# Optimization experiments

Measured on AMD Instinct MI355X. Metric: run time of the kernel, lower is better.

## Reference

```python
import jax, jax.numpy as jnp
import numpy as np

NUM_POINTS = 16384
OVERSAMPLE = 3
IMPORTANCE_RATIO = 0.75


def point_sample(feat, coords):
    """grid_sample(bilinear, align_corners=False, zero padding) at [0,1]^2 coords.
    feat: (N, C, H, W); coords: (N, P, 2) with coords[...,0]=x (width), [...,1]=y.
    Returns (N, C, P)."""
    N, C, H, W = feat.shape
    # grid_sample with g = 2c-1, align_corners=False -> pixel = c*size - 0.5
    x = coords[..., 0] * W - 0.5
    y = coords[..., 1] * H - 0.5
    x0 = jnp.floor(x)
    y0 = jnp.floor(y)
    x1 = x0 + 1.0
    y1 = y0 + 1.0
    wx1 = x - x0
    wx0 = 1.0 - wx1
    wy1 = y - y0
    wy0 = 1.0 - wy1
    featf = feat.reshape(N, C, H * W)

    def gather(yi, xi):
        valid = (xi >= 0) & (xi <= W - 1) & (yi >= 0) & (yi <= H - 1)
        xic = jnp.clip(xi, 0, W - 1).astype(jnp.int32)
        yic = jnp.clip(yi, 0, H - 1).astype(jnp.int32)
        idx = yic * W + xic  # (N, P)
        v = jnp.take_along_axis(featf, idx[:, None, :], axis=2)  # (N, C, P)
        return v * valid[:, None, :].astype(feat.dtype)

    out = (gather(y0, x0) * (wy0 * wx0)[:, None, :]
           + gather(y0, x1) * (wy0 * wx1)[:, None, :]
           + gather(y1, x0) * (wy1 * wx0)[:, None, :]
           + gather(y1, x1) * (wy1 * wx1)[:, None, :])
    return out


def calculate_uncertainty(logits):
    """logits: (N, C, P) -> (N, P) uncertainty = top2 - top1 (<= 0)."""
    if logits.shape[1] == 1:
        return -jnp.abs(logits)[:, 0, :]
    top2 = jax.lax.top_k(jnp.moveaxis(logits, 1, -1), 2)[0]  # (N, P, 2)
    return top2[..., 1] - top2[..., 0]


def sample_point_coords(coarse_logits):
    """get_uncertain_point_coords_with_randomness (torch.no_grad branch)."""
    N = coarse_logits.shape[0]
    num_sampled = NUM_POINTS * OVERSAMPLE
    num_imp = int(IMPORTANCE_RATIO * NUM_POINTS)
    num_rand = NUM_POINTS - num_imp
    k1, k2 = jax.random.split(jax.random.key(7))
    cand = jax.random.uniform(k1, (N, num_sampled, 2), dtype=jnp.float32)
    cand_logits = point_sample(coarse_logits, cand)  # (N, C, S)
    unc = calculate_uncertainty(cand_logits)  # (N, S)
    idx = jax.lax.top_k(unc, num_imp)[1]  # (N, num_imp)
    imp = jnp.take_along_axis(cand, idx[..., None], axis=1)  # (N, num_imp, 2)
    rand = jax.random.uniform(k2, (N, num_rand, 2), dtype=jnp.float32)
    return jnp.concatenate([imp, rand], axis=1)  # (N, P, 2)


def point_head(fine, coarse_pts, w0, b0, w1, b1, w2, b2, wp, bp):
    x = jnp.concatenate([fine, coarse_pts], axis=1)  # (N, nin+C, P)
    for w, b in ((w0, b0), (w1, b1), (w2, b2)):
        x = jax.nn.relu(jnp.einsum('oc,ncp->nop', w, x) + b[None, :, None])
        x = jnp.concatenate([x, coarse_pts], axis=1)  # coarse_pred_each_layer
    return jnp.einsum('oc,ncp->nop', wp, x) + bp[None, :, None]  # (N, C, P)


def setup_inputs() -> dict:
    key = jax.random.key(0)
    ks = jax.random.split(key, 8)
    N, C, Hc, Wc = 8, 19, 64, 64
    nin, Hf, Wf = 256, 128, 128
    fin = nin + C  # 275
    return {
        'coarse_sem_seg_logits': jax.random.normal(ks[0], (N, C, Hc, Wc), jnp.float32),
        'features': jax.random.normal(ks[1], (N, nin, Hf, Wf), jnp.float32),
        'w0': jax.random.normal(ks[2], (nin, fin), jnp.float32) * (2.0 / fin) ** 0.5,
        'b0': jnp.zeros((nin,), jnp.float32),
        'w1': jax.random.normal(ks[3], (nin, fin), jnp.float32) * (2.0 / fin) ** 0.5,
        'b1': jnp.zeros((nin,), jnp.float32),
        'w2': jax.random.normal(ks[4], (nin, fin), jnp.float32) * (2.0 / fin) ** 0.5,
        'b2': jnp.zeros((nin,), jnp.float32),
        'wp': jax.random.normal(ks[5], (C, fin), jnp.float32) * 0.001,
        'bp': jnp.zeros((C,), jnp.float32),
    }


def reference(coarse_sem_seg_logits, features, w0, b0, w1, b1, w2, b2, wp, bp):
    # training-mode forward of PointRendSemSegHead
    point_coords = jax.lax.stop_gradient(
        sample_point_coords(jax.lax.stop_gradient(coarse_sem_seg_logits)))
    coarse_pts = point_sample(coarse_sem_seg_logits, point_coords)  # (N, C, P)
    fine_pts = point_sample(features, point_coords)  # (N, nin, P)
    point_logits = point_head(fine_pts, coarse_pts, w0, b0, w1, b1, w2, b2, wp, bp)
    return coarse_sem_seg_logits, point_logits, point_coords
```

## Files before the change

### kernel.cpp

```cpp
#include <hip/hip_runtime.h>
#include <stdint.h>

#pragma clang fp contract(off)

#define NB    8
#define CCH   19
#define FCH   256
#define FIN   275
#define KP    288
#define NPTS  16384
#define NSAMP 49152
#define NIMP  12288
#define NRAND 4096
#define SORT_M 65536
#define CHUNK  8192
#define TP    64
#define XROW  640
#define WBF_OFF (4u << 20)
#define FTR_OFF (8u << 20)
#define FTR_BYTES (134217728ull / 2)

typedef __attribute__((ext_vector_type(8))) short bf16x8;
typedef __attribute__((ext_vector_type(4))) float f32x4;

__host__ __device__ __forceinline__ uint32_t rotl32(uint32_t v, int r) {
  return (v << r) | (v >> (32 - r));
}

__host__ __device__ __forceinline__ void tf2x32(uint32_t k0, uint32_t k1,
                                                uint32_t x0, uint32_t x1,
                                                uint32_t* o0, uint32_t* o1) {
  const uint32_t ks2 = k0 ^ k1 ^ 0x1BD11BDAu;
  x0 += k0; x1 += k1;
#define TF_R(r) { x0 += x1; x1 = rotl32(x1, (r)); x1 ^= x0; }
  TF_R(13) TF_R(15) TF_R(26) TF_R(6)
  x0 += k1;  x1 += ks2 + 1u;
  TF_R(17) TF_R(29) TF_R(16) TF_R(24)
  x0 += ks2; x1 += k0 + 2u;
  TF_R(13) TF_R(15) TF_R(26) TF_R(6)
  x0 += k0;  x1 += k1 + 3u;
  TF_R(17) TF_R(29) TF_R(16) TF_R(24)
  x0 += k1;  x1 += ks2 + 4u;
  TF_R(13) TF_R(15) TF_R(26) TF_R(6)
  x0 += ks2; x1 += k0 + 5u;
#undef TF_R
  *o0 = x0; *o1 = x1;
}

__device__ __forceinline__ float u01_at(uint32_t k0, uint32_t k1, uint32_t i) {
  uint32_t o0, o1;
  tf2x32(k0, k1, 0u, i, &o0, &o1);
  const uint32_t b = o0 ^ o1;
  const float f = __uint_as_float((b >> 9) | 0x3f800000u) - 1.0f;
  return fmaxf(0.0f, f);
}

__device__ __forceinline__ unsigned short f2bf(float f) {
  const uint32_t u = __float_as_uint(f);
  return (unsigned short)((u + 0x7fffu + ((u >> 16) & 1u)) >> 16);
}

__device__ __forceinline__ float bf2f(unsigned short h) {
  return __uint_as_float((uint32_t)h << 16);
}

template <int SZ>
__device__ __forceinline__ void interp(float cx, float cy, int* off, float* wgt) {
  const float X = cx * (float)SZ - 0.5f, Y = cy * (float)SZ - 0.5f;
  const float x0f = floorf(X), y0f = floorf(Y);
  const float fx = X - x0f, fy = Y - y0f;
  const float wx0 = 1.0f - fx, wy0 = 1.0f - fy;
  const int x0 = (int)x0f, y0 = (int)y0f;
  const int x0c = min(max(x0, 0), SZ - 1), x1c = min(max(x0 + 1, 0), SZ - 1);
  const int y0c = min(max(y0, 0), SZ - 1), y1c = min(max(y0 + 1, 0), SZ - 1);
  const bool vx0 = (x0 >= 0) & (x0 <= SZ - 1), vx1 = (x0 >= -1) & (x0 <= SZ - 2);
  const bool vy0 = (y0 >= 0) & (y0 <= SZ - 1), vy1 = (y0 >= -1) & (y0 <= SZ - 2);
  off[0] = y0c * SZ + x0c; wgt[0] = (vy0 & vx0) ? wy0 * wx0 : 0.0f;
  off[1] = y0c * SZ + x1c; wgt[1] = (vy0 & vx1) ? wy0 * fx  : 0.0f;
  off[2] = y1c * SZ + x0c; wgt[2] = (vy1 & vx0) ? fy  * wx0 : 0.0f;
  off[3] = y1c * SZ + x1c; wgt[3] = (vy1 & vx1) ? fy  * fx  : 0.0f;
}

__global__ __launch_bounds__(256) void fusedA(
    const float* __restrict__ feats, unsigned short* __restrict__ ftr,
    const float* __restrict__ coarse, unsigned long long* __restrict__ keys,
    const float* __restrict__ w0, const float* __restrict__ w1,
    const float* __restrict__ w2, const float* __restrict__ wpw,
    unsigned short* __restrict__ wbf, unsigned short* __restrict__ wpb,
    uint32_t k1a, uint32_t k1b, int use_tr) {
  __shared__ unsigned short tile[64][66];
  const int bid = blockIdx.x;
  const int t = threadIdx.x;

  if (bid < 8192) {
    if (!use_tr) return;
    const int nn = bid >> 10;
    const int ct = (bid >> 8) & 3;
    const int pt = bid & 255;
    const int c0 = ct * 64, p0 = pt * 64;
    const float* src = feats + ((size_t)nn << 22);
#pragma unroll 4
    for (int k = 0; k < 16; ++k) {
      const int c = 4 * k + (t >> 6);
      const int p = t & 63;
      tile[p][c] = f2bf(src[((size_t)(c0 + c) << 14) + p0 + p]);
    }
    __syncthreads();
    const int p = t >> 2, q = t & 3;
    const int cb = q * 16;
    uint32_t w[8];
#pragma unroll
    for (int m = 0; m < 8; ++m)
      w[m] = (uint32_t)tile[p][cb + 2 * m] | ((uint32_t)tile[p][cb + 2 * m + 1] << 16);
    unsigned short* dst = ftr + ((((size_t)nn << 14) + p0 + p) << 8) + c0 + cb;
    *(uint4*)(dst)     = make_uint4(w[0], w[1], w[2], w[3]);
    *(uint4*)(dst + 8) = make_uint4(w[4], w[5], w[6], w[7]);
  } else if (bid < 10240) {
    const int tid = (bid - 8192) * 256 + t;
    const int nn = tid >> 16, s = tid & (SORT_M - 1);
    if (s >= NSAMP) { keys[tid] = 0xFFFFFFFFFFFFFFFFull; return; }
    const uint32_t ci = (uint32_t)(((unsigned)nn * NSAMP + (unsigned)s) * 2);
    const float cx = u01_at(k1a, k1b, ci);
    const float cy = u01_at(k1a, k1b, ci + 1);
    const float X = cx * 64.0f - 0.5f, Y = cy * 64.0f - 0.5f;
    const float x0f = floorf(X), y0f = floorf(Y);
    const float fx = X - x0f, fy = Y - y0f;
    const float wx0 = 1.0f - fx, wy0 = 1.0f - fy;
    const int x0 = (int)x0f, y0 = (int)y0f;
    const int x0c = min(max(x0, 0), 63), x1c = min(max(x0 + 1, 0), 63);
    const int y0c = min(max(y0, 0), 63), y1c = min(max(y0 + 1, 0), 63);
    const bool vx0 = (x0 >= 0) & (x0 <= 63), vx1 = (x0 >= -1) & (x0 <= 62);
    const bool vy0 = (y0 >= 0) & (y0 <= 63), vy1 = (y0 >= -1) & (y0 <= 62);
    const float w00 = (vy0 & vx0) ? wy0 * wx0 : 0.0f;
    const float w01 = (vy0 & vx1) ? wy0 * fx  : 0.0f;
    const float w10 = (vy1 & vx0) ? fy  * wx0 : 0.0f;
    const float w11 = (vy1 & vx1) ? fy  * fx  : 0.0f;
    const int o00 = y0c * 64 + x0c, o01 = y0c * 64 + x1c;
    const int o10 = y1c * 64 + x0c, o11 = y1c * 64 + x1c;
    const float* cb = coarse + (size_t)nn * (CCH * 4096);
    float m1 = -3.402823466e38f, m2 = -3.402823466e38f;
    for (int c = 0; c < CCH; ++c) {
      const float* pch = cb + (size_t)c * 4096;
      const float v = ((pch[o00] * w00 + pch[o01] * w01) + pch[o10] * w10) + pch[o11] * w11;
      if (v > m1) { m2 = m1; m1 = v; } else if (v > m2) { m2 = v; }
    }
    const float unc = m2 - m1;
    const uint32_t b = __float_as_uint(unc);
    const uint32_t asc = (b & 0x80000000u) ? ~b : (b | 0x80000000u);
    keys[tid] = ((unsigned long long)(~asc) << 32) | (uint32_t)s;
  } else {
    const int i = (bid - 10240) * 256 + t;
    if (i < 3 * 256 * KP) {
      const int L = i / (256 * KP);
      const int rem = i - L * (256 * KP);
      const int o = rem / KP, k = rem - o * KP;
      const float* W = (L == 0) ? w0 : (L == 1) ? w1 : w2;
      wbf[i] = (k < FIN) ? f2bf(W[o * FIN + k]) : (unsigned short)0;
    } else {
      const int j = i - 3 * 256 * KP;
      const int o = j / KP, k = j - o * KP;
      wpb[j] = (o < CCH && k < FIN) ? f2bf(wpw[o * FIN + k]) : (unsigned short)0;
    }
  }
}

__global__ __launch_bounds__(1024) void bitonic_local(unsigned long long* __restrict__ keys) {
  __shared__ unsigned long long s[CHUNK];
  const int cb = blockIdx.x;
  unsigned long long* a = keys + (size_t)cb * CHUNK;
  const unsigned gbase = (unsigned)(cb * CHUNK) & (SORT_M - 1);
  for (int i = threadIdx.x; i < CHUNK; i += 1024) s[i] = a[i];
  __syncthreads();
  for (int k = 2; k <= CHUNK; k <<= 1) {
    for (int j = k >> 1; j > 0; j >>= 1) {
      for (int pid = threadIdx.x; pid < CHUNK / 2; pid += 1024) {
        const int i = ((pid & ~(j - 1)) << 1) | (pid & (j - 1));
        const int l = i | j;
        const bool up = (((gbase + i) & k) == 0);
        const unsigned long long x = s[i], y = s[l];
        if ((x > y) == up) { s[i] = y; s[l] = x; }
      }
      __syncthreads();
    }
  }
  for (int i = threadIdx.x; i < CHUNK; i += 1024) a[i] = s[i];
}

__global__ __launch_bounds__(256) void bitonic_global(unsigned long long* __restrict__ keys,
                                                      int k, int j, int ppb_shift) {
  const int t = blockIdx.x * blockDim.x + threadIdx.x;
  const int b = t >> ppb_shift, pid = t & ((1 << ppb_shift) - 1);
  const int i = ((pid & ~(j - 1)) << 1) | (pid & (j - 1));
  const int l = i | j;
  const bool up = ((i & k) == 0);
  unsigned long long* a = keys + ((size_t)b << 16);
  const unsigned long long x = a[i], y = a[l];
  if ((x > y) == up) { a[i] = y; a[l] = x; }
}

__global__ __launch_bounds__(1024) void bitonic_finish(unsigned long long* __restrict__ keys,
                                                       int k) {
  __shared__ unsigned long long s[CHUNK];
  const int cb = blockIdx.x;
  unsigned long long* a = keys + (size_t)cb * CHUNK;
  const unsigned gi0 = (unsigned)(cb * CHUNK) & (SORT_M - 1);
  for (int i = threadIdx.x; i < CHUNK; i += 1024) s[i] = a[i];
  __syncthreads();
  const bool up = ((gi0 & k) == 0);
  for (int j = CHUNK >> 1; j > 0; j >>= 1) {
    for (int pid = threadIdx.x; pid < CHUNK / 2; pid += 1024) {
      const int i = ((pid & ~(j - 1)) << 1) | (pid & (j - 1));
      const int l = i | j;
      const unsigned long long x = s[i], y = s[l];
      if ((x > y) == up) { s[i] = y; s[l] = x; }
    }
    __syncthreads();
  }
  for (int i = threadIdx.x; i < CHUNK; i += 1024) a[i] = s[i];
}

__global__ __launch_bounds__(1024) void finlow_coords(
    const unsigned long long* __restrict__ keys, float* __restrict__ outc,
    uint32_t k1a, uint32_t k1b, uint32_t k2a, uint32_t k2b) {
  __shared__ unsigned long long s[CHUNK];
  const int nn = blockIdx.x >> 1, half = blockIdx.x & 1;
  const unsigned long long* a = keys + ((size_t)nn << 16) + half * CHUNK;
  for (int i = threadIdx.x; i < CHUNK; i += 1024) s[i] = a[i];
  __syncthreads();
  for (int j = CHUNK >> 1; j > 0; j >>= 1) {
    for (int pid = threadIdx.x; pid < CHUNK / 2; pid += 1024) {
      const int i = ((pid & ~(j - 1)) << 1) | (pid & (j - 1));
      const int l = i | j;
      const unsigned long long x = s[i], y = s[l];
      if (x > y) { s[i] = y; s[l] = x; }
    }
    __syncthreads();
  }
  const int pb = half * CHUNK;
  for (int q = threadIdx.x; q < CHUNK; q += 1024) {
    const int p = pb + q;
    float cx, cy;
    if (p < NIMP) {
      const unsigned idx = (unsigned)(s[q] & 0xFFFFFFFFu);
      const uint32_t ci = ((unsigned)nn * NSAMP + idx) * 2;
      cx = u01_at(k1a, k1b, ci);
      cy = u01_at(k1a, k1b, ci + 1);
    } else {
      const uint32_t ri = ((unsigned)nn * NRAND + (unsigned)(p - NIMP)) * 2;
      cx = u01_at(k2a, k2b, ri);
      cy = u01_at(k2a, k2b, ri + 1);
    }
    float* o = outc + (((size_t)nn << 14) + p) * 2;
    o[0] = cx; o[1] = cy;
  }
}

template <int USE_TR>
__global__ __launch_bounds__(512, 4) void fused_mfma(
    const float* __restrict__ coarse, const float* __restrict__ feats,
    const unsigned short* __restrict__ ftr,
    const float* __restrict__ b0, const float* __restrict__ b1,
    const float* __restrict__ b2, const float* __restrict__ bp,
    const unsigned short* __restrict__ wbf, const unsigned short* __restrict__ wpb,
    const float* __restrict__ pc, float* __restrict__ outl) {
  __shared__ __align__(16) unsigned short xp[TP * (XROW / 2)];

  const int t = threadIdx.x;
  const int nn = blockIdx.x >> 8;
  const int pbase = (blockIdx.x & 255) * TP;

  int offF[4]; float wgtF[4];
  int offC[4]; float wgtC[4];
  int offFc[4]; float wgtFc[4];
  {
    const float2 c = *(const float2*)(pc + ((size_t)nn * NPTS + pbase + (t >> 3)) * 2);
    interp<128>(c.x, c.y, offF, wgtF);
  }
  {
    const float2 c = *(const float2*)(pc + ((size_t)nn * NPTS + pbase + (t & 63)) * 2);
    interp<64>(c.x, c.y, offC, wgtC);
    if (!USE_TR) interp<128>(c.x, c.y, offFc, wgtFc);
  }

  if (USE_TR) {
    const int p = t >> 3, q = t & 7;
    const unsigned short* base = ftr + (((size_t)nn << 14) << 8) + q * 32;
    const unsigned short* n0 = base + ((size_t)offF[0] << 8);
    const unsigned short* n1 = base + ((size_t)offF[1] << 8);
    const unsigned short* n2 = base + ((size_t)offF[2] << 8);
    const unsigned short* n3 = base + ((size_t)offF[3] << 8);
    const float g0 = wgtF[0], g1 = wgtF[1], g2 = wgtF[2], g3 = wgtF[3];
    const unsigned swzp = (unsigned)(p & 7) << 4;
#pragma unroll
    for (int m = 0; m < 4; ++m) {
      const bf16x8 a = *(const bf16x8*)(n0 + m * 8);
      const bf16x8 bq = *(const bf16x8*)(n1 + m * 8);
      const bf16x8 c = *(const bf16x8*)(n2 + m * 8);
      const bf16x8 d = *(const bf16x8*)(n3 + m * 8);
      uint32_t u[4];
#pragma unroll
      for (int e = 0; e < 4; ++e) {
        float v0 = fmaf(bf2f((unsigned short)a[2 * e]), g0,
                   fmaf(bf2f((unsigned short)bq[2 * e]), g1,
                   fmaf(bf2f((unsigned short)c[2 * e]), g2,
                        bf2f((unsigned short)d[2 * e]) * g3)));
        float v1 = fmaf(bf2f((unsigned short)a[2 * e + 1]), g0,
                   fmaf(bf2f((unsigned short)bq[2 * e + 1]), g1,
                   fmaf(bf2f((unsigned short)c[2 * e + 1]), g2,
                        bf2f((unsigned short)d[2 * e + 1]) * g3)));
        u[e] = (uint32_t)f2bf(v0) | ((uint32_t)f2bf(v1) << 16);
      }
      *(uint4*)((char*)xp + p * XROW + (((unsigned)((q * 32 + m * 8) * 2)) ^ swzp)) =
          make_uint4(u[0], u[1], u[2], u[3]);
    }
  }

  for (int i = (USE_TR ? 8192 : 0) + t; i < (KP / 2) * TP; i += 512) {
    const int p = i & (TP - 1);
    const int c0 = (i >> 6) * 2;
    float v0 = 0.0f, v1 = 0.0f;
    if (!USE_TR && c0 < FCH) {
      const float* fb0 = feats + ((size_t)nn << 22) + ((size_t)c0 << 14);
      const float* fb1 = fb0 + 16384;
      v0 = ((fb0[offFc[0]] * wgtFc[0] + fb0[offFc[1]] * wgtFc[1])
           + fb0[offFc[2]] * wgtFc[2]) + fb0[offFc[3]] * wgtFc[3];
      v1 = ((fb1[offFc[0]] * wgtFc[0] + fb1[offFc[1]] * wgtFc[1])
           + fb1[offFc[2]] * wgtFc[2]) + fb1[offFc[3]] * wgtFc[3];
    } else if (c0 >= FCH && c0 < FIN) {
      const float* cb0 = coarse + (size_t)nn * (CCH * 4096) + (size_t)(c0 - FCH) * 4096;
      v0 = ((cb0[offC[0]] * wgtC[0] + cb0[offC[1]] * wgtC[1])
           + cb0[offC[2]] * wgtC[2]) + cb0[offC[3]] * wgtC[3];
      if (c0 + 1 < FIN) {
        const float* cb1 = cb0 + 4096;
        v1 = ((cb1[offC[0]] * wgtC[0] + cb1[offC[1]] * wgtC[1])
             + cb1[offC[2]] * wgtC[2]) + cb1[offC[3]] * wgtC[3];
      }
    }
    const uint32_t u = (uint32_t)f2bf(v0) | ((uint32_t)f2bf(v1) << 16);
    *(uint32_t*)((char*)xp + p * XROW + (((unsigned)(c0 * 2)) ^ ((unsigned)(p & 7) << 4))) = u;
  }

  const int lane = t & 63, wave = t >> 6;
  const int wm = wave & 3, wn = wave >> 2;
  const int l15 = lane & 15, g = lane >> 4;
  const unsigned swz = (unsigned)(l15 & 7) << 4;
  const char* xpB = (const char*)xp;

#pragma unroll
  for (int L = 0; L < 3; ++L) {
    __syncthreads();
    const float* Bv = (L == 0) ? b0 : (L == 1) ? b1 : b2;
    const unsigned short* wL = wbf + (size_t)L * (256 * KP);
    const unsigned short* wbase = wL + (size_t)(wm * 64 + l15) * KP + g * 8;

    f32x4 acc[4][2];
#pragma unroll
    for (int mt = 0; mt < 4; ++mt)
#pragma unroll
      for (int nt = 0; nt < 2; ++nt) acc[mt][nt] = (f32x4)(0.0f);

    for (int ks = 0; ks < 9; ++ks) {
      const bf16x8 a0 = *(const bf16x8*)(wbase + 0 * 16 * KP + ks * 32);
      const bf16x8 a1 = *(const bf16x8*)(wbase + 1 * 16 * KP + ks * 32);
      const bf16x8 a2 = *(const bf16x8*)(wbase + 2 * 16 * KP + ks * 32);
      const bf16x8 a3 = *(const bf16x8*)(wbase + 3 * 16 * KP + ks * 32);
      const unsigned kb = (unsigned)(ks * 64 + g * 16) ^ swz;
      const bf16x8 q0 = *(const bf16x8*)(xpB + (wn * 32 + 0 + l15) * XROW + kb);
      const bf16x8 q1 = *(const bf16x8*)(xpB + (wn * 32 + 16 + l15) * XROW + kb);
      acc[0][0] = __builtin_amdgcn_mfma_f32_16x16x32_bf16(a0, q0, acc[0][0], 0, 0, 0);
      acc[1][0] = __builtin_amdgcn_mfma_f32_16x16x32_bf16(a1, q0, acc[1][0], 0, 0, 0);
      acc[2][0] = __builtin_amdgcn_mfma_f32_16x16x32_bf16(a2, q0, acc[2][0], 0, 0, 0);
      acc[3][0] = __builtin_amdgcn_mfma_f32_16x16x32_bf16(a3, q0, acc[3][0], 0, 0, 0);
      acc[0][1] = __builtin_amdgcn_mfma_f32_16x16x32_bf16(a0, q1, acc[0][1], 0, 0, 0);
      acc[1][1] = __builtin_amdgcn_mfma_f32_16x16x32_bf16(a1, q1, acc[1][1], 0, 0, 0);
      acc[2][1] = __builtin_amdgcn_mfma_f32_16x16x32_bf16(a2, q1, acc[2][1], 0, 0, 0);
      acc[3][1] = __builtin_amdgcn_mfma_f32_16x16x32_bf16(a3, q1, acc[3][1], 0, 0, 0);
    }
    __syncthreads();

#pragma unroll
    for (int mt = 0; mt < 4; ++mt) {
      const int ch0 = wm * 64 + mt * 16 + (g << 2);
      const float4 bv = *(const float4*)(Bv + ch0);
#pragma unroll
      for (int nt = 0; nt < 2; ++nt) {
        const int p = wn * 32 + nt * 16 + l15;
        const f32x4 v = acc[mt][nt];
        const unsigned short h0 = f2bf(fmaxf(v[0] + bv.x, 0.0f));
        const unsigned short h1 = f2bf(fmaxf(v[1] + bv.y, 0.0f));
        const unsigned short h2 = f2bf(fmaxf(v[2] + bv.z, 0.0f));
        const unsigned short h3 = f2bf(fmaxf(v[3] + bv.w, 0.0f));
        uint2 u;
        u.x = (uint32_t)h0 | ((uint32_t)h1 << 16);
        u.y = (uint32_t)h2 | ((uint32_t)h3 << 16);
        *(uint2*)((char*)xp + p * XROW + (((unsigned)(ch0 * 2)) ^ swz)) = u;
      }
    }
  }
  __syncthreads();

  const int hmt = wave >> 2, hnt = wave & 3;
  const unsigned short* hbase = wpb + (size_t)(hmt * 16 + l15) * KP + g * 8;
  f32x4 hacc = (f32x4)(0.0f);
  for (int ks = 0; ks < 9; ++ks) {
    const unsigned kb = (unsigned)(ks * 64 + g * 16) ^ swz;
    const bf16x8 ha = *(const bf16x8*)(hbase + ks * 32);
    const bf16x8 hb = *(const bf16x8*)(xpB + (hnt * 16 + l15) * XROW + kb);
    hacc = __builtin_amdgcn_mfma_f32_16x16x32_bf16(ha, hb, hacc, 0, 0, 0);
  }
  const int p = pbase + hnt * 16 + l15;
#pragma unroll
  for (int j = 0; j < 4; ++j) {
    const int ch = hmt * 16 + (g << 2) + j;
    if (ch < CCH)
      outl[((size_t)nn * CCH + ch) * NPTS + p] = hacc[j] + bp[ch];
  }
}

extern "C" void kernel_launch(void* const* d_in, const int* in_sizes, int n_in,
                              void* d_out, int out_size, void* d_ws, size_t ws_size,
                              hipStream_t stream) {
  const float* coarse = (const float*)d_in[0];
  const float* feats  = (const float*)d_in[1];
  const float* w0 = (const float*)d_in[2]; const float* b0 = (const float*)d_in[3];
  const float* w1 = (const float*)d_in[4]; const float* b1 = (const float*)d_in[5];
  const float* w2 = (const float*)d_in[6]; const float* b2 = (const float*)d_in[7];
  const float* wp = (const float*)d_in[8]; const float* bp = (const float*)d_in[9];

  float* out0 = (float*)d_out;
  float* outL = out0 + 622592;
  float* outC = outL + 2490368;

  unsigned long long* keys = (unsigned long long*)d_ws;
  unsigned short* wbf = (unsigned short*)((char*)d_ws + WBF_OFF);
  unsigned short* wpb = wbf + 3 * 256 * KP;
  unsigned short* ftr = (unsigned short*)((char*)d_ws + FTR_OFF);
  const int use_tr = (ws_size >= (size_t)FTR_OFF + FTR_BYTES) ? 1 : 0;

  uint32_t k1a, k1b, k2a, k2b;
  tf2x32(0u, 7u, 0u, 0u, &k1a, &k1b);
  tf2x32(0u, 7u, 0u, 1u, &k2a, &k2b);

  hipMemcpyAsync(out0, coarse, 622592 * sizeof(float),
                 hipMemcpyDeviceToDevice, stream);

  fusedA<<<11140, 256, 0, stream>>>(feats, ftr, coarse, keys,
                                    w0, w1, w2, wp, wbf, wpb, k1a, k1b, use_tr);

  bitonic_local<<<64, 1024, 0, stream>>>(keys);
  bitonic_global<<<1024, 256, 0, stream>>>(keys, 16384, 8192, 15);
  bitonic_finish<<<64, 1024, 0, stream>>>(keys, 16384);
  bitonic_global<<<1024, 256, 0, stream>>>(keys, 32768, 16384, 15);
  bitonic_global<<<1024, 256, 0, stream>>>(keys, 32768, 8192, 15);
  bitonic_finish<<<64, 1024, 0, stream>>>(keys, 32768);
  bitonic_global<<<1024, 256, 0, stream>>>(keys, 65536, 32768, 15);
  bitonic_global<<<512, 256, 0, stream>>>(keys, 65536, 16384, 14);
  bitonic_global<<<256, 256, 0, stream>>>(keys, 65536, 8192, 13);
  finlow_coords<<<16, 1024, 0, stream>>>(keys, outC, k1a, k1b, k2a, k2b);

  if (use_tr)
    fused_mfma<1><<<2048, 512, 0, stream>>>(coarse, feats, ftr, b0, b1, b2, bp,
                                            wbf, wpb, outC, outL);
  else
    fused_mfma<0><<<2048, 512, 0, stream>>>(coarse, feats, ftr, b0, b1, b2, bp,
                                            wbf, wpb, outC, outL);
}
```

Baseline: 389.3 us.

## Transpose coarse logits to pixel-major and double MFMA point tile to 128

Adds a kernel that transposes the coarse logits into a channel-padded pixel-major buffer. Both the uncertainty pass and the MLP's coarse-feature gather can then use vectorized 16-byte loads per corner instead of 19 strided scalar loads. The fused MFMA kernel now processes 128 points per block with a 4x4 accumulator tile, which gives more weight reuse per block. The cost is half the grid size and lower occupancy (launch bounds go from 4 to 2), plus one extra small launch and a workspace buffer.

```diff
diff --git a/kernel.cpp b/kernel.cpp
--- a/kernel.cpp
+++ b/kernel.cpp
@@ -5,6 +5,7 @@
 
 #define NB    8
 #define CCH   19
+#define CSTR  20
 #define FCH   256
 #define FIN   275
 #define KP    288
@@ -14,9 +15,10 @@
 #define NRAND 4096
 #define SORT_M 65536
 #define CHUNK  8192
-#define TP    64
+#define TP    128
 #define XROW  640
 #define WBF_OFF (4u << 20)
+#define CTR_OFF (4718592u)
 #define FTR_OFF (8u << 20)
 #define FTR_BYTES (134217728ull / 2)
 
@@ -81,9 +83,31 @@
   off[3] = y1c * SZ + x1c; wgt[3] = (vy1 & vx1) ? fy  * fx  : 0.0f;
 }
 
+__global__ __launch_bounds__(256) void ctr_transpose(
+    const float* __restrict__ coarse, float* __restrict__ ctr) {
+  __shared__ float tile[CCH][257];
+  const int b = blockIdx.x;
+  const int nn = b >> 4, px0 = (b & 15) * 256;
+  const int t = threadIdx.x;
+  const float* src = coarse + (size_t)nn * (CCH * 4096) + px0;
+#pragma unroll
+  for (int c = 0; c < CCH; ++c) tile[c][t] = src[c * 4096 + t];
+  __syncthreads();
+  float v[CSTR];
+#pragma unroll
+  for (int c = 0; c < CCH; ++c) v[c] = tile[c][t];
+  v[19] = 0.0f;
+  float* dst = ctr + ((size_t)(nn << 12) + px0 + t) * CSTR;
+#pragma unroll
+  for (int k = 0; k < 5; ++k) {
+    f32x4 x; x[0] = v[4*k]; x[1] = v[4*k+1]; x[2] = v[4*k+2]; x[3] = v[4*k+3];
+    *(f32x4*)(dst + 4 * k) = x;
+  }
+}
+
 __global__ __launch_bounds__(256) void fusedA(
     const float* __restrict__ feats, unsigned short* __restrict__ ftr,
-    const float* __restrict__ coarse, unsigned long long* __restrict__ keys,
+    const float* __restrict__ ctr, unsigned long long* __restrict__ keys,
     const float* __restrict__ w0, const float* __restrict__ w1,
     const float* __restrict__ w2, const float* __restrict__ wpw,
     unsigned short* __restrict__ wbf, unsigned short* __restrict__ wpb,
@@ -135,14 +159,26 @@
     const float w01 = (vy0 & vx1) ? wy0 * fx  : 0.0f;
     const float w10 = (vy1 & vx0) ? fy  * wx0 : 0.0f;
     const float w11 = (vy1 & vx1) ? fy  * fx  : 0.0f;
-    const int o00 = y0c * 64 + x0c, o01 = y0c * 64 + x1c;
-    const int o10 = y1c * 64 + x0c, o11 = y1c * 64 + x1c;
-    const float* cb = coarse + (size_t)nn * (CCH * 4096);
+    const float* rb = ctr + ((size_t)nn << 12) * CSTR;
+    const float* r0 = rb + (size_t)(y0c * 64 + x0c) * CSTR;
+    const float* r1 = rb + (size_t)(y0c * 64 + x1c) * CSTR;
+    const float* r2 = rb + (size_t)(y1c * 64 + x0c) * CSTR;
+    const float* r3 = rb + (size_t)(y1c * 64 + x1c) * CSTR;
     float m1 = -3.402823466e38f, m2 = -3.402823466e38f;
-    for (int c = 0; c < CCH; ++c) {
-      const float* pch = cb + (size_t)c * 4096;
-      const float v = ((pch[o00] * w00 + pch[o01] * w01) + pch[o10] * w10) + pch[o11] * w11;
-      if (v > m1) { m2 = m1; m1 = v; } else if (v > m2) { m2 = v; }
+#pragma unroll
+    for (int k = 0; k < 5; ++k) {
+      const f32x4 x0v = *(const f32x4*)(r0 + 4 * k);
+      const f32x4 x1v = *(const f32x4*)(r1 + 4 * k);
+      const f32x4 x2v = *(const f32x4*)(r2 + 4 * k);
+      const f32x4 x3v = *(const f32x4*)(r3 + 4 * k);
+#pragma unroll
+      for (int e = 0; e < 4; ++e) {
+        const int c = 4 * k + e;
+        if (c < CCH) {
+          const float v = ((x0v[e] * w00 + x1v[e] * w01) + x2v[e] * w10) + x3v[e] * w11;
+          if (v > m1) { m2 = m1; m1 = v; } else if (v > m2) { m2 = v; }
+        }
+      }
     }
     const float unc = m2 - m1;
     const uint32_t b = __float_as_uint(unc);
@@ -256,9 +292,9 @@
 }
 
 template <int USE_TR>
-__global__ __launch_bounds__(512, 4) void fused_mfma(
+__global__ __launch_bounds__(512, 2) void fused_mfma(
     const float* __restrict__ coarse, const float* __restrict__ feats,
-    const unsigned short* __restrict__ ftr,
+    const unsigned short* __restrict__ ftr, const float* __restrict__ ctr,
     const float* __restrict__ b0, const float* __restrict__ b1,
     const float* __restrict__ b2, const float* __restrict__ bp,
     const unsigned short* __restrict__ wbf, const unsigned short* __restrict__ wpb,
@@ -266,25 +302,25 @@
   __shared__ __align__(16) unsigned short xp[TP * (XROW / 2)];
 
   const int t = threadIdx.x;
-  const int nn = blockIdx.x >> 8;
-  const int pbase = (blockIdx.x & 255) * TP;
+  const int nn = blockIdx.x >> 7;
+  const int pbase = (blockIdx.x & 127) * TP;
 
   int offF[4]; float wgtF[4];
   int offC[4]; float wgtC[4];
   int offFc[4]; float wgtFc[4];
   {
-    const float2 c = *(const float2*)(pc + ((size_t)nn * NPTS + pbase + (t >> 3)) * 2);
+    const float2 c = *(const float2*)(pc + ((size_t)nn * NPTS + pbase + (t >> 2)) * 2);
     interp<128>(c.x, c.y, offF, wgtF);
   }
   {
-    const float2 c = *(const float2*)(pc + ((size_t)nn * NPTS + pbase + (t & 63)) * 2);
+    const float2 c = *(const float2*)(pc + ((size_t)nn * NPTS + pbase + (t & 127)) * 2);
     interp<64>(c.x, c.y, offC, wgtC);
     if (!USE_TR) interp<128>(c.x, c.y, offFc, wgtFc);
   }
 
   if (USE_TR) {
-    const int p = t >> 3, q = t & 7;
-    const unsigned short* base = ftr + (((size_t)nn << 14) << 8) + q * 32;
+    const int p = t >> 2, q = t & 3;
+    const unsigned short* base = ftr + ((size_t)nn << 22) + q * 64;
     const unsigned short* n0 = base + ((size_t)offF[0] << 8);
     const unsigned short* n1 = base + ((size_t)offF[1] << 8);
     const unsigned short* n2 = base + ((size_t)offF[2] << 8);
@@ -292,7 +328,7 @@
     const float g0 = wgtF[0], g1 = wgtF[1], g2 = wgtF[2], g3 = wgtF[3];
     const unsigned swzp = (unsigned)(p & 7) << 4;
 #pragma unroll
-    for (int m = 0; m < 4; ++m) {
+    for (int m = 0; m < 8; ++m) {
       const bf16x8 a = *(const bf16x8*)(n0 + m * 8);
       const bf16x8 bq = *(const bf16x8*)(n1 + m * 8);
       const bf16x8 c = *(const bf16x8*)(n2 + m * 8);
@@ -310,34 +346,70 @@
                         bf2f((unsigned short)d[2 * e + 1]) * g3)));
         u[e] = (uint32_t)f2bf(v0) | ((uint32_t)f2bf(v1) << 16);
       }
-      *(uint4*)((char*)xp + p * XROW + (((unsigned)((q * 32 + m * 8) * 2)) ^ swzp)) =
+      *(uint4*)((char*)xp + p * XROW + (((unsigned)(q * 128 + m * 16)) ^ swzp)) =
           make_uint4(u[0], u[1], u[2], u[3]);
     }
-  }
-
-  for (int i = (USE_TR ? 8192 : 0) + t; i < (KP / 2) * TP; i += 512) {
-    const int p = i & (TP - 1);
-    const int c0 = (i >> 6) * 2;
-    float v0 = 0.0f, v1 = 0.0f;
-    if (!USE_TR && c0 < FCH) {
-      const float* fb0 = feats + ((size_t)nn << 22) + ((size_t)c0 << 14);
-      const float* fb1 = fb0 + 16384;
-      v0 = ((fb0[offFc[0]] * wgtFc[0] + fb0[offFc[1]] * wgtFc[1])
-           + fb0[offFc[2]] * wgtFc[2]) + fb0[offFc[3]] * wgtFc[3];
-      v1 = ((fb1[offFc[0]] * wgtFc[0] + fb1[offFc[1]] * wgtFc[1])
-           + fb1[offFc[2]] * wgtFc[2]) + fb1[offFc[3]] * wgtFc[3];
-    } else if (c0 >= FCH && c0 < FIN) {
-      const float* cb0 = coarse + (size_t)nn * (CCH * 4096) + (size_t)(c0 - FCH) * 4096;
-      v0 = ((cb0[offC[0]] * wgtC[0] + cb0[offC[1]] * wgtC[1])
-           + cb0[offC[2]] * wgtC[2]) + cb0[offC[3]] * wgtC[3];
-      if (c0 + 1 < FIN) {
-        const float* cb1 = cb0 + 4096;
-        v1 = ((cb1[offC[0]] * wgtC[0] + cb1[offC[1]] * wgtC[1])
-             + cb1[offC[2]] * wgtC[2]) + cb1[offC[3]] * wgtC[3];
-      }
-    }
-    const uint32_t u = (uint32_t)f2bf(v0) | ((uint32_t)f2bf(v1) << 16);
-    *(uint32_t*)((char*)xp + p * XROW + (((unsigned)(c0 * 2)) ^ ((unsigned)(p & 7) << 4))) = u;
+    if (t < TP) {
+      const int pp = t;
+      const float* rb = ctr + ((size_t)nn << 12) * CSTR;
+      const float* r0 = rb + (size_t)offC[0] * CSTR;
+      const float* r1 = rb + (size_t)offC[1] * CSTR;
+      const float* r2 = rb + (size_t)offC[2] * CSTR;
+      const float* r3 = rb + (size_t)offC[3] * CSTR;
+      const float h0 = wgtC[0], h1 = wgtC[1], h2 = wgtC[2], h3 = wgtC[3];
+      unsigned short hs[32];
+#pragma unroll
+      for (int k = 0; k < 5; ++k) {
+        const f32x4 x0v = *(const f32x4*)(r0 + 4 * k);
+        const f32x4 x1v = *(const f32x4*)(r1 + 4 * k);
+        const f32x4 x2v = *(const f32x4*)(r2 + 4 * k);
+        const f32x4 x3v = *(const f32x4*)(r3 + 4 * k);
+#pragma unroll
+        for (int e = 0; e < 4; ++e) {
+          const int c = 4 * k + e;
+          if (c < CCH)
+            hs[c] = f2bf(fmaf(x0v[e], h0, fmaf(x1v[e], h1,
+                         fmaf(x2v[e], h2, x3v[e] * h3))));
+        }
+      }
+#pragma unroll
+      for (int c = CCH; c < 32; ++c) hs[c] = 0;
+      const unsigned swzc = (unsigned)(pp & 7) << 4;
+#pragma unroll
+      for (int k = 0; k < 4; ++k) {
+        uint4 u;
+        u.x = (uint32_t)hs[8*k]   | ((uint32_t)hs[8*k+1] << 16);
+        u.y = (uint32_t)hs[8*k+2] | ((uint32_t)hs[8*k+3] << 16);
+        u.z = (uint32_t)hs[8*k+4] | ((uint32_t)hs[8*k+5] << 16);
+        u.w = (uint32_t)hs[8*k+6] | ((uint32_t)hs[8*k+7] << 16);
+        *(uint4*)((char*)xp + pp * XROW + (((unsigned)(512 + 16 * k)) ^ swzc)) = u;
+      }
+    }
+  } else {
+    for (int i = t; i < (KP / 2) * TP; i += 512) {
+      const int p = i & (TP - 1);
+      const int c0 = (i >> 7) * 2;
+      float v0 = 0.0f, v1 = 0.0f;
+      if (c0 < FCH) {
+        const float* fb0 = feats + ((size_t)nn << 22) + ((size_t)c0 << 14);
+        const float* fb1 = fb0 + 16384;
+        v0 = ((fb0[offFc[0]] * wgtFc[0] + fb0[offFc[1]] * wgtFc[1])
+             + fb0[offFc[2]] * wgtFc[2]) + fb0[offFc[3]] * wgtFc[3];
+        v1 = ((fb1[offFc[0]] * wgtFc[0] + fb1[offFc[1]] * wgtFc[1])
+             + fb1[offFc[2]] * wgtFc[2]) + fb1[offFc[3]] * wgtFc[3];
+      } else if (c0 < FIN) {
+        const float* cb0 = coarse + (size_t)nn * (CCH * 4096) + (size_t)(c0 - FCH) * 4096;
+        v0 = ((cb0[offC[0]] * wgtC[0] + cb0[offC[1]] * wgtC[1])
+             + cb0[offC[2]] * wgtC[2]) + cb0[offC[3]] * wgtC[3];
+        if (c0 + 1 < FIN) {
+          const float* cb1 = cb0 + 4096;
+          v1 = ((cb1[offC[0]] * wgtC[0] + cb1[offC[1]] * wgtC[1])
+               + cb1[offC[2]] * wgtC[2]) + cb1[offC[3]] * wgtC[3];
+        }
+      }
+      const uint32_t u = (uint32_t)f2bf(v0) | ((uint32_t)f2bf(v1) << 16);
+      *(uint32_t*)((char*)xp + p * XROW + (((unsigned)(c0 * 2)) ^ ((unsigned)(p & 7) << 4))) = u;
+    }
   }
 
   const int lane = t & 63, wave = t >> 6;
@@ -353,11 +425,11 @@
     const unsigned short* wL = wbf + (size_t)L * (256 * KP);
     const unsigned short* wbase = wL + (size_t)(wm * 64 + l15) * KP + g * 8;
 
-    f32x4 acc[4][2];
+    f32x4 acc[4][4];
 #pragma unroll
     for (int mt = 0; mt < 4; ++mt)
 #pragma unroll
-      for (int nt = 0; nt < 2; ++nt) acc[mt][nt] = (f32x4)(0.0f);
+      for (int nt = 0; nt < 4; ++nt) acc[mt][nt] = (f32x4)(0.0f);
 
     for (int ks = 0; ks < 9; ++ks) {
       const bf16x8 a0 = *(const bf16x8*)(wbase + 0 * 16 * KP + ks * 32);
@@ -365,16 +437,18 @@
       const bf16x8 a2 = *(const bf16x8*)(wbase + 2 * 16 * KP + ks * 32);
       const bf16x8 a3 = *(const bf16x8*)(wbase + 3 * 16 * KP + ks * 32);
       const unsigned kb = (unsigned)(ks * 64 + g * 16) ^ swz;
-      const bf16x8 q0 = *(const bf16x8*)(xpB + (wn * 32 + 0 + l15) * XROW + kb);
-      const bf16x8 q1 = *(const bf16x8*)(xpB + (wn * 32 + 16 + l15) * XROW + kb);
-      acc[0][0] = __builtin_amdgcn_mfma_f32_16x16x32_bf16(a0, q0, acc[0][0], 0, 0, 0);
-      acc[1][0] = __builtin_amdgcn_mfma_f32_16x16x32_bf16(a1, q0, acc[1][0], 0, 0, 0);
-      acc[2][0] = __builtin_amdgcn_mfma_f32_16x16x32_bf16(a2, q0, acc[2][0], 0, 0, 0);
-      acc[3][0] = __builtin_amdgcn_mfma_f32_16x16x32_bf16(a3, q0, acc[3][0], 0, 0, 0);
-      acc[0][1] = __builtin_amdgcn_mfma_f32_16x16x32_bf16(a0, q1, acc[0][1], 0, 0, 0);
-      acc[1][1] = __builtin_amdgcn_mfma_f32_16x16x32_bf16(a1, q1, acc[1][1], 0, 0, 0);
-      acc[2][1] = __builtin_amdgcn_mfma_f32_16x16x32_bf16(a2, q1, acc[2][1], 0, 0, 0);
-      acc[3][1] = __builtin_amdgcn_mfma_f32_16x16x32_bf16(a3, q1, acc[3][1], 0, 0, 0);
+      const bf16x8 q0 = *(const bf16x8*)(xpB + (wn * 64 +  0 + l15) * XROW + kb);
+      const bf16x8 q1 = *(const bf16x8*)(xpB + (wn * 64 + 16 + l15) * XROW + kb);
+      const bf16x8 q2 = *(const bf16x8*)(xpB + (wn * 64 + 32 + l15) * XROW + kb);
+      const bf16x8 q3 = *(const bf16x8*)(xpB + (wn * 64 + 48 + l15) * XROW + kb);
+#pragma unroll
+      for (int nt = 0; nt < 4; ++nt) {
+        const bf16x8 bq = (nt == 0) ? q0 : (nt == 1) ? q1 : (nt == 2) ? q2 : q3;
+        acc[0][nt] = __builtin_amdgcn_mfma_f32_16x16x32_bf16(a0, bq, acc[0][nt], 0, 0, 0);
+        acc[1][nt] = __builtin_amdgcn_mfma_f32_16x16x32_bf16(a1, bq, acc[1][nt], 0, 0, 0);
+        acc[2][nt] = __builtin_amdgcn_mfma_f32_16x16x32_bf16(a2, bq, acc[2][nt], 0, 0, 0);
+        acc[3][nt] = __builtin_amdgcn_mfma_f32_16x16x32_bf16(a3, bq, acc[3][nt], 0, 0, 0);
+      }
     }
     __syncthreads();
 
@@ -383,8 +457,8 @@
       const int ch0 = wm * 64 + mt * 16 + (g << 2);
       const float4 bv = *(const float4*)(Bv + ch0);
 #pragma unroll
-      for (int nt = 0; nt < 2; ++nt) {
-        const int p = wn * 32 + nt * 16 + l15;
+      for (int nt = 0; nt < 4; ++nt) {
+        const int p = wn * 64 + nt * 16 + l15;
         const f32x4 v = acc[mt][nt];
         const unsigned short h0 = f2bf(fmaxf(v[0] + bv.x, 0.0f));
         const unsigned short h1 = f2bf(fmaxf(v[1] + bv.y, 0.0f));
@@ -399,21 +473,25 @@
   }
   __syncthreads();
 
-  const int hmt = wave >> 2, hnt = wave & 3;
-  const unsigned short* hbase = wpb + (size_t)(hmt * 16 + l15) * KP + g * 8;
-  f32x4 hacc = (f32x4)(0.0f);
+  const unsigned short* hb0 = wpb + (size_t)l15 * KP + g * 8;
+  const unsigned short* hb1 = wpb + (size_t)(16 + l15) * KP + g * 8;
+  f32x4 hacc0 = (f32x4)(0.0f), hacc1 = (f32x4)(0.0f);
   for (int ks = 0; ks < 9; ++ks) {
     const unsigned kb = (unsigned)(ks * 64 + g * 16) ^ swz;
-    const bf16x8 ha = *(const bf16x8*)(hbase + ks * 32);
-    const bf16x8 hb = *(const bf16x8*)(xpB + (hnt * 16 + l15) * XROW + kb);
-    hacc = __builtin_amdgcn_mfma_f32_16x16x32_bf16(ha, hb, hacc, 0, 0, 0);
-  }
-  const int p = pbase + hnt * 16 + l15;
+    const bf16x8 hbq = *(const bf16x8*)(xpB + (wave * 16 + l15) * XROW + kb);
+    const bf16x8 ha0 = *(const bf16x8*)(hb0 + ks * 32);
+    const bf16x8 ha1 = *(const bf16x8*)(hb1 + ks * 32);
+    hacc0 = __builtin_amdgcn_mfma_f32_16x16x32_bf16(ha0, hbq, hacc0, 0, 0, 0);
+    hacc1 = __builtin_amdgcn_mfma_f32_16x16x32_bf16(ha1, hbq, hacc1, 0, 0, 0);
+  }
+  const int p = pbase + wave * 16 + l15;
 #pragma unroll
   for (int j = 0; j < 4; ++j) {
-    const int ch = hmt * 16 + (g << 2) + j;
-    if (ch < CCH)
-      outl[((size_t)nn * CCH + ch) * NPTS + p] = hacc[j] + bp[ch];
+    const int ch0 = (g << 2) + j;
+    outl[((size_t)nn * CCH + ch0) * NPTS + p] = hacc0[j] + bp[ch0];
+    const int ch1 = 16 + (g << 2) + j;
+    if (ch1 < CCH)
+      outl[((size_t)nn * CCH + ch1) * NPTS + p] = hacc1[j] + bp[ch1];
   }
 }
 
@@ -434,6 +512,7 @@
   unsigned long long* keys = (unsigned long long*)d_ws;
   unsigned short* wbf = (unsigned short*)((char*)d_ws + WBF_OFF);
   unsigned short* wpb = wbf + 3 * 256 * KP;
+  float* ctr = (float*)((char*)d_ws + CTR_OFF);
   unsigned short* ftr = (unsigned short*)((char*)d_ws + FTR_OFF);
   const int use_tr = (ws_size >= (size_t)FTR_OFF + FTR_BYTES) ? 1 : 0;
 
@@ -444,7 +523,9 @@
   hipMemcpyAsync(out0, coarse, 622592 * sizeof(float),
                  hipMemcpyDeviceToDevice, stream);
 
-  fusedA<<<11140, 256, 0, stream>>>(feats, ftr, coarse, keys,
+  ctr_transpose<<<128, 256, 0, stream>>>(coarse, ctr);
+
+  fusedA<<<11140, 256, 0, stream>>>(feats, ftr, ctr, keys,
                                     w0, w1, w2, wp, wbf, wpb, k1a, k1b, use_tr);
 
   bitonic_local<<<64, 1024, 0, stream>>>(keys);
@@ -459,9 +540,9 @@
   finlow_coords<<<16, 1024, 0, stream>>>(keys, outC, k1a, k1b, k2a, k2b);
 
   if (use_tr)
-    fused_mfma<1><<<2048, 512, 0, stream>>>(coarse, feats, ftr, b0, b1, b2, bp,
-                                            wbf, wpb, outC, outL);
+    fused_mfma<1><<<1024, 512, 0, stream>>>(coarse, feats, ftr, ctr, b0, b1, b2,
+                                            bp, wbf, wpb, outC, outL);
   else
-    fused_mfma<0><<<2048, 512, 0, stream>>>(coarse, feats, ftr, b0, b1, b2, bp,
-                                            wbf, wpb, outC, outL);
-}
+    fused_mfma<0><<<1024, 512, 0, stream>>>(coarse, feats, ftr, ctr, b0, b1, b2,
+                                            bp, wbf, wpb, outC, outL);
+}
```

Result: slower. 398.3 us (+2.3%).
